# Performance work log

Measured on AMD Instinct MI355X. Metric: run time of the kernel, lower is better.

## Reference

```python
import jax, jax.numpy as jnp
import numpy as np

N_FIELDS = 8
N_NODES = 100000
N_EDGES = 6400000


def setup_inputs() -> dict:
    key = jax.random.key(0)
    k1, k2, k3, k4, k5 = jax.random.split(key, 5)
    q = jax.random.normal(k1, (N_FIELDS, N_NODES), dtype=jnp.float32)
    edges = jax.random.normal(k2, (N_EDGES, 1), dtype=jnp.float32)
    senders = jax.random.randint(k3, (N_EDGES,), 0, N_NODES, dtype=jnp.int32)
    receivers = jax.random.randint(k4, (N_EDGES,), 0, N_NODES, dtype=jnp.int32)
    dt = jax.random.uniform(k5, (1,), dtype=jnp.float32)
    # learned parameters, initialized exactly as in DeltaQGNN.__init__
    w_self = jnp.linspace(0.05, 0.09, N_FIELDS)
    w_msg = jnp.linspace(0.02, 0.04, N_FIELDS)
    w_edge = jnp.linspace(0.01, 0.03, N_FIELDS)
    b = jnp.linspace(0.005, 0.008, N_FIELDS)
    return {"q": q, "edges": edges, "senders": senders, "receivers": receivers,
            "dt": dt, "w_self": w_self, "w_msg": w_msg, "w_edge": w_edge, "b": b}


def reference(q, edges, senders, receivers, dt, w_self, w_msg, w_edge, b):
    # q: [F, N], edges: [E, 1], senders/receivers: [E], dt: [1]
    n_nodes = q.shape[1]
    edge_scalar = edges[:, 0]                                    # [E]
    # gather sender values for all fields at once: [F, E]
    msg_in = q[:, senders] + w_edge[:, None] * edge_scalar[None, :]
    # scatter-add to receivers per field: [F, N]
    msg = jax.vmap(lambda m: jax.ops.segment_sum(m, receivers, num_segments=n_nodes))(msg_in)
    rhs = w_self[:, None] * q + w_msg[:, None] * msg + b[:, None]
    return dt * rhs                                              # [F, N]
```

## Files before the change

kernel.cpp:

```cpp
#include <hip/hip_runtime.h>

#define NF 8
#define BSHIFT 8
#define BNODES 256
#define MAXNB 512
#define TPB 256
#define TPR 512
#define TPBF 1024
#define CHUNKF 6144
#define KPE 6
#define NBLKF 512
#define CAPB 17408
#define SPLIT 8
#define CAP 24
#define IDXSTR 26
#define LSLICE 2560

__global__ void k_transpose(const float* __restrict__ q, float* __restrict__ qT,
                            float* __restrict__ govf, unsigned* __restrict__ gcur,
                            int n_nodes, int nb) {
    int n = blockIdx.x * blockDim.x + threadIdx.x;
    if (n < nb) gcur[n] = 0u;
    if (n >= n_nodes) return;
    float4 a, b;
    a.x = q[0 * n_nodes + n]; a.y = q[1 * n_nodes + n];
    a.z = q[2 * n_nodes + n]; a.w = q[3 * n_nodes + n];
    b.x = q[4 * n_nodes + n]; b.y = q[5 * n_nodes + n];
    b.z = q[6 * n_nodes + n]; b.w = q[7 * n_nodes + n];
    float4* dst = reinterpret_cast<float4*>(qT + (size_t)n * NF);
    dst[0] = a; dst[1] = b;
    float* o = govf + (size_t)n * 9;
#pragma unroll
    for (int k = 0; k < 9; ++k) o[k] = 0.f;
}

__global__ __launch_bounds__(TPBF) void k_scatter_fused(
        const float* __restrict__ edges, const int* __restrict__ senders,
        const int* __restrict__ receivers, int n_edges, int nb, int tiles,
        unsigned* __restrict__ gcur, const float* __restrict__ qT,
        float* __restrict__ govf, uint2* __restrict__ rec) {
    __shared__ uint2 lrec[CHUNKF];
    __shared__ unsigned short lbkt[CHUNKF];
    __shared__ unsigned hist[MAXNB];
    __shared__ unsigned lbase[MAXNB];
    __shared__ unsigned gbase[MAXNB];

    for (int t = blockIdx.x; t < tiles; t += gridDim.x) {
        int start = t * CHUNKF;
        int end = min(start + CHUNKF, n_edges);
        int n = end - start;

        for (int i = threadIdx.x; i < nb; i += TPBF) hist[i] = 0u;
        __syncthreads();

        unsigned rcx[KPE], rcy[KPE], meta[KPE];
#pragma unroll
        for (int k = 0; k < KPE; ++k) {
            int i = (int)threadIdx.x + k * TPBF;
            meta[k] = 0xFFFFFFFFu;
            if (i < n) {
                int e = start + i;
                int s = senders[e];
                int r = receivers[e];
                float ev = edges[e];
                unsigned bkt = (unsigned)r >> BSHIFT;
                unsigned p = atomicAdd(&hist[bkt], 1u);
                rcx[k] = ((unsigned)(r & (BNODES - 1)) << 17) | (unsigned)s;
                rcy[k] = __float_as_uint(ev);
                meta[k] = (p << 9) | bkt;
            }
        }
        __syncthreads();

        if (threadIdx.x < (unsigned)nb)
            gbase[threadIdx.x] = atomicAdd(&gcur[threadIdx.x], hist[threadIdx.x]);
        if (threadIdx.x < 64) {
            int lane = threadIdx.x;
            unsigned carry = 0;
            for (int base = 0; base < nb; base += 64) {
                int bi = base + lane;
                unsigned v = (bi < nb) ? hist[bi] : 0u;
                unsigned x = v;
                for (int d = 1; d < 64; d <<= 1) {
                    unsigned y = __shfl_up(x, d, 64);
                    if (lane >= d) x += y;
                }
                if (bi < nb) lbase[bi] = carry + x - v;
                carry += __shfl(x, 63, 64);
            }
        }
        __syncthreads();

#pragma unroll
        for (int k = 0; k < KPE; ++k) {
            if (meta[k] != 0xFFFFFFFFu) {
                unsigned bkt = meta[k] & 0x1FFu;
                unsigned p   = meta[k] >> 9;
                unsigned slot = lbase[bkt] + p;
                lrec[slot] = make_uint2(rcx[k], rcy[k]);
                lbkt[slot] = (unsigned short)bkt;
            }
        }
        __syncthreads();

        for (int j = threadIdx.x; j < n; j += TPBF) {
            unsigned bkt = lbkt[j];
            uint2 rc = lrec[j];
            unsigned off = gbase[bkt] + ((unsigned)j - lbase[bkt]);
            if (off < CAPB) {
                rec[(size_t)bkt * CAPB + off] = rc;
            } else {
                unsigned snd = rc.x & 0x1FFFFu;
                unsigned rl = rc.x >> 17;
                float ev = __uint_as_float(rc.y);
                const float4* qs = reinterpret_cast<const float4*>(qT + (size_t)snd * NF);
                float4 q0 = qs[0];
                float4 q1 = qs[1];
                float* a = govf + ((size_t)bkt * BNODES + rl) * 9;
                atomicAdd(a + 0, q0.x); atomicAdd(a + 1, q0.y);
                atomicAdd(a + 2, q0.z); atomicAdd(a + 3, q0.w);
                atomicAdd(a + 4, q1.x); atomicAdd(a + 5, q1.y);
                atomicAdd(a + 6, q1.z); atomicAdd(a + 7, q1.w);
                atomicAdd(a + 8, ev);
            }
        }
        __syncthreads();
    }
}

__global__ __launch_bounds__(TPR) void k_reduce_slot(
        const uint2* __restrict__ rec, const unsigned* __restrict__ gcur,
        const float* __restrict__ qT, float* __restrict__ part,
        float* __restrict__ govf, int n_nodes) {
    __shared__ uint2 lrec[LSLICE];
    __shared__ unsigned short idx[BNODES * IDXSTR];
    __shared__ unsigned cur[BNODES];
    int t = threadIdx.x;
    if (t < BNODES) cur[t] = 0;
    __syncthreads();

    int bkt = blockIdx.x / SPLIT;
    int s   = blockIdx.x % SPLIT;
    unsigned len = gcur[bkt];
    if (len > CAPB) len = CAPB;
    size_t base = (size_t)bkt * CAPB;
    unsigned a0 = (unsigned)(((unsigned long long)len * s) / SPLIT);
    unsigned a1 = (unsigned)(((unsigned long long)len * (s + 1)) / SPLIT);
    unsigned slice = a1 - a0;

    for (unsigned i = t; i < slice; i += TPR) {
        uint2 rc = rec[base + a0 + i];
        if (i < LSLICE) lrec[i] = rc;
        unsigned rl = rc.x >> 17;
        unsigned pos = atomicAdd(&cur[rl], 1u);
        if (pos < CAP) {
            idx[rl * IDXSTR + pos] = (unsigned short)i;
        } else {
            unsigned snd = rc.x & 0x1FFFFu;
            float ev = __uint_as_float(rc.y);
            const float4* qs = reinterpret_cast<const float4*>(qT + (size_t)snd * NF);
            float4 q0 = qs[0];
            float4 q1 = qs[1];
            float* a = govf + ((size_t)bkt * BNODES + rl) * 9;
            atomicAdd(a + 0, q0.x); atomicAdd(a + 1, q0.y);
            atomicAdd(a + 2, q0.z); atomicAdd(a + 3, q0.w);
            atomicAdd(a + 4, q1.x); atomicAdd(a + 5, q1.y);
            atomicAdd(a + 6, q1.z); atomicAdd(a + 7, q1.w);
            atomicAdd(a + 8, ev);
        }
    }
    __syncthreads();

    int node = t >> 1;
    int parity = t & 1;
    float m[9];
#pragma unroll
    for (int k = 0; k < 9; ++k) m[k] = 0.f;
    unsigned cntv = cur[node];
    if (cntv > CAP) cntv = CAP;
    for (unsigned j = parity; j < cntv; j += 2) {
        unsigned i0 = idx[node * IDXSTR + j];
        uint2 rc0 = (i0 < LSLICE) ? lrec[i0] : rec[base + a0 + i0];
        const float4* qs0 = reinterpret_cast<const float4*>(qT + (size_t)(rc0.x & 0x1FFFFu) * NF);
        float4 a0v = qs0[0], a1v = qs0[1];
        m[0] += a0v.x; m[1] += a0v.y; m[2] += a0v.z; m[3] += a0v.w;
        m[4] += a1v.x; m[5] += a1v.y; m[6] += a1v.z; m[7] += a1v.w;
        m[8] += __uint_as_float(rc0.y);
    }
    __syncthreads();

    float* scratch = reinterpret_cast<float*>(lrec);
    if (parity == 1) {
        float* d = scratch + (size_t)node * 9;
#pragma unroll
        for (int k = 0; k < 9; ++k) d[k] = m[k];
    }
    __syncthreads();
    if (parity == 0) {
        const float* p2 = scratch + (size_t)node * 9;
        float* dst = part + (size_t)blockIdx.x * (BNODES * 9) + (size_t)node * 9;
#pragma unroll
        for (int k = 0; k < 9; ++k) dst[k] = m[k] + p2[k];
    }
}

__global__ void k_finalize2(const float* __restrict__ part, const float* __restrict__ govf,
                            const float* __restrict__ q,
                            const float* __restrict__ dtp, const float* __restrict__ w_self,
                            const float* __restrict__ w_msg, const float* __restrict__ w_edge,
                            const float* __restrict__ bv, float* __restrict__ out,
                            int split, int n_nodes) {
    int n = blockIdx.x * blockDim.x + threadIdx.x;
    if (n >= n_nodes) return;
    int bkt = n >> BSHIFT;
    int rl = n & (BNODES - 1);
    float m[9];
#pragma unroll
    for (int f = 0; f < 9; ++f) m[f] = govf[(size_t)n * 9 + f];
    for (int s = 0; s < split; ++s) {
        const float* p = part + ((size_t)(bkt * split + s) * BNODES + rl) * 9;
#pragma unroll
        for (int f = 0; f < 9; ++f) m[f] += p[f];
    }
    float dtv = dtp[0];
    float evs = m[8];
#pragma unroll
    for (int f = 0; f < NF; ++f) {
        float msg = m[f] + w_edge[f] * evs;
        out[(size_t)f * n_nodes + n] =
            dtv * (w_self[f] * q[(size_t)f * n_nodes + n] + w_msg[f] * msg + bv[f]);
    }
}

__global__ void k_transpose_zero(const float* __restrict__ q, float* __restrict__ qT,
                                 float* __restrict__ msgT, int n_nodes) {
    int n = blockIdx.x * blockDim.x + threadIdx.x;
    if (n >= n_nodes) return;
    float v[NF];
#pragma unroll
    for (int f = 0; f < NF; ++f) v[f] = q[f * n_nodes + n];
    float4* dst = reinterpret_cast<float4*>(qT + (size_t)n * NF);
    dst[0] = make_float4(v[0], v[1], v[2], v[3]);
    dst[1] = make_float4(v[4], v[5], v[6], v[7]);
    float4 z = make_float4(0.f, 0.f, 0.f, 0.f);
    float4* m = reinterpret_cast<float4*>(msgT + (size_t)n * NF);
    m[0] = z; m[1] = z;
}

__global__ void k_edge_scatter(const float* __restrict__ edges, const int* __restrict__ senders,
                               const int* __restrict__ receivers, const float* __restrict__ qT,
                               float* __restrict__ msgT, const float* __restrict__ w_edge,
                               int n_edges) {
    float we[NF];
#pragma unroll
    for (int f = 0; f < NF; ++f) we[f] = w_edge[f];
    int idx = blockIdx.x * blockDim.x + threadIdx.x;
    int stride = gridDim.x * blockDim.x;
    for (int e = idx; e < n_edges; e += stride) {
        int s = senders[e];
        int r = receivers[e];
        float ev = edges[e];
        const float4* qs = reinterpret_cast<const float4*>(qT + (size_t)s * NF);
        float4 q0 = qs[0];
        float4 q1 = qs[1];
        float* m = msgT + (size_t)r * NF;
        atomicAdd(m + 0, q0.x + we[0] * ev);
        atomicAdd(m + 1, q0.y + we[1] * ev);
        atomicAdd(m + 2, q0.z + we[2] * ev);
        atomicAdd(m + 3, q0.w + we[3] * ev);
        atomicAdd(m + 4, q1.x + we[4] * ev);
        atomicAdd(m + 5, q1.y + we[5] * ev);
        atomicAdd(m + 6, q1.z + we[6] * ev);
        atomicAdd(m + 7, q1.w + we[7] * ev);
    }
}

__global__ void k_finalize(const float* __restrict__ q, const float* __restrict__ msgT,
                           const float* __restrict__ dt, const float* __restrict__ w_self,
                           const float* __restrict__ w_msg, const float* __restrict__ b,
                           float* __restrict__ out, int n_nodes) {
    int n = blockIdx.x * blockDim.x + threadIdx.x;
    if (n >= n_nodes) return;
    float dtv = dt[0];
    const float4* m4 = reinterpret_cast<const float4*>(msgT + (size_t)n * NF);
    float4 m0 = m4[0];
    float4 m1 = m4[1];
    float mv[NF] = {m0.x, m0.y, m0.z, m0.w, m1.x, m1.y, m1.z, m1.w};
#pragma unroll
    for (int f = 0; f < NF; ++f) {
        out[f * n_nodes + n] = dtv * (w_self[f] * q[f * n_nodes + n] + w_msg[f] * mv[f] + b[f]);
    }
}

extern "C" void kernel_launch(void* const* d_in, const int* in_sizes, int n_in,
                              void* d_out, int out_size, void* d_ws, size_t ws_size,
                              hipStream_t stream) {
    const float* q         = (const float*)d_in[0];
    const float* edges     = (const float*)d_in[1];
    const int*   senders   = (const int*)d_in[2];
    const int*   receivers = (const int*)d_in[3];
    const float* dt        = (const float*)d_in[4];
    const float* w_self    = (const float*)d_in[5];
    const float* w_msg     = (const float*)d_in[6];
    const float* w_edge    = (const float*)d_in[7];
    const float* b         = (const float*)d_in[8];
    float* out = (float*)d_out;

    const int n_nodes = in_sizes[0] / NF;
    const int n_edges = in_sizes[2];
    const int nb = (n_nodes + BNODES - 1) >> BSHIFT;
    const int tiles = (n_edges + CHUNKF - 1) / CHUNKF;

    size_t rec_bytes  = (size_t)nb * CAPB * 8;
    size_t qT_bytes   = (size_t)n_nodes * NF * 4;
    size_t gcur_bytes = 256 + (size_t)nb * 4;
    size_t govf_bytes = (size_t)nb * BNODES * 9 * 4;
    size_t part_bytes = (size_t)SPLIT * nb * BNODES * 9 * 4;
    size_t need = rec_bytes + qT_bytes + gcur_bytes + govf_bytes + part_bytes + 1024;

    double mean_per_bucket = (double)n_edges / (double)nb;
    bool ok = (n_nodes <= 131072) && (nb <= MAXNB) && (need <= ws_size) &&
              (mean_per_bucket + 8.0 * __builtin_sqrt(mean_per_bucket) < (double)CAPB);

    if (ok) {
        char* p = (char*)d_ws;
        uint2*    rec  = (uint2*)p;    p += rec_bytes;
        float*    qT   = (float*)p;    p += qT_bytes;
        unsigned* gcur = (unsigned*)p; p += gcur_bytes;
        float*    govf = (float*)p;    p += govf_bytes;
        float*    part = (float*)(((uintptr_t)p + 255) & ~(uintptr_t)255);

        int nblk_f = tiles < NBLKF ? tiles : NBLKF;

        k_transpose<<<(n_nodes + TPB - 1) / TPB, TPB, 0, stream>>>(q, qT, govf, gcur,
                                                                   n_nodes, nb);
        k_scatter_fused<<<nblk_f, TPBF, 0, stream>>>(edges, senders, receivers, n_edges,
                                                     nb, tiles, gcur, qT, govf, rec);
        k_reduce_slot<<<nb * SPLIT, TPR, 0, stream>>>(rec, gcur, qT, part, govf, n_nodes);
        k_finalize2<<<(n_nodes + TPB - 1) / TPB, TPB, 0, stream>>>(
            part, govf, q, dt, w_self, w_msg, w_edge, b, out, SPLIT, n_nodes);
    } else {
        float* qT   = (float*)d_ws;
        float* msgT = qT + (size_t)n_nodes * NF;
        k_transpose_zero<<<(n_nodes + TPB - 1) / TPB, TPB, 0, stream>>>(q, qT, msgT, n_nodes);
        k_edge_scatter<<<3072, TPB, 0, stream>>>(edges, senders, receivers, qT, msgT,
                                                 w_edge, n_edges);
        k_finalize<<<(n_nodes + TPB - 1) / TPB, TPB, 0, stream>>>(q, msgT, dt, w_self, w_msg,
                                                                  b, out, n_nodes);
    }
}
```

Measured before the change: 108.6 us.

## Stage reduce-slot records via direct global-to-LDS loads and retune scatter blocks

The reduce kernel now copies each slice's records into shared memory with the asynchronous global_load_lds builtin in 1 KB wave chunks before processing, instead of loading them through registers and storing them to LDS inside the loop. Slice boundaries are rounded to even indices so the 16-byte copies stay aligned, and the last slice takes the remainder. The scatter kernel is retuned to smaller blocks with smaller chunks and more blocks, and the workspace padding grows. The copy can read up to one 1 KB chunk past the slice end, which relies on that padding and adds a full barrier before processing.

```diff
diff --git a/kernel.cpp b/kernel.cpp
--- a/kernel.cpp
+++ b/kernel.cpp
@@ -6,10 +6,10 @@
 #define MAXNB 512
 #define TPB 256
 #define TPR 512
-#define TPBF 1024
-#define CHUNKF 6144
+#define TPBF 512
+#define CHUNKF 3072
 #define KPE 6
-#define NBLKF 512
+#define NBLKF 1024
 #define CAPB 17408
 #define SPLIT 8
 #define CAP 24
@@ -132,25 +132,59 @@
         const uint2* __restrict__ rec, const unsigned* __restrict__ gcur,
         const float* __restrict__ qT, float* __restrict__ part,
         float* __restrict__ govf, int n_nodes) {
-    __shared__ uint2 lrec[LSLICE];
+    __shared__ __align__(16) uint2 lrec[LSLICE];
     __shared__ unsigned short idx[BNODES * IDXSTR];
     __shared__ unsigned cur[BNODES];
     int t = threadIdx.x;
     if (t < BNODES) cur[t] = 0;
-    __syncthreads();
 
     int bkt = blockIdx.x / SPLIT;
     int s   = blockIdx.x % SPLIT;
     unsigned len = gcur[bkt];
     if (len > CAPB) len = CAPB;
     size_t base = (size_t)bkt * CAPB;
-    unsigned a0 = (unsigned)(((unsigned long long)len * s) / SPLIT);
-    unsigned a1 = (unsigned)(((unsigned long long)len * (s + 1)) / SPLIT);
+    unsigned a0 = ((unsigned)(((unsigned long long)len * s) / SPLIT)) & ~1u;
+    unsigned a1 = (s + 1 == SPLIT) ? len
+                : ((unsigned)(((unsigned long long)len * (s + 1)) / SPLIT)) & ~1u;
     unsigned slice = a1 - a0;
-
-    for (unsigned i = t; i < slice; i += TPR) {
+    unsigned staged = slice < LSLICE ? slice : LSLICE;
+
+    {
+        int wid = t >> 6, lane = t & 63;
+        unsigned ncalls = (staged * 8u + 1023u) >> 10;
+        const char* g0 = (const char*)(rec + base + a0);
+        for (unsigned c = wid; c < ncalls; c += TPR / 64) {
+            const char* g = g0 + (size_t)c * 1024 + (size_t)lane * 16;
+            char* l = (char*)lrec + (size_t)c * 1024;
+            __builtin_amdgcn_global_load_lds(
+                (const __attribute__((address_space(1))) void*)g,
+                (__attribute__((address_space(3))) void*)l, 16, 0, 0);
+        }
+    }
+    __syncthreads();
+
+    for (unsigned i = t; i < staged; i += TPR) {
+        uint2 rc = lrec[i];
+        unsigned rl = rc.x >> 17;
+        unsigned pos = atomicAdd(&cur[rl], 1u);
+        if (pos < CAP) {
+            idx[rl * IDXSTR + pos] = (unsigned short)i;
+        } else {
+            unsigned snd = rc.x & 0x1FFFFu;
+            float ev = __uint_as_float(rc.y);
+            const float4* qs = reinterpret_cast<const float4*>(qT + (size_t)snd * NF);
+            float4 q0 = qs[0];
+            float4 q1 = qs[1];
+            float* a = govf + ((size_t)bkt * BNODES + rl) * 9;
+            atomicAdd(a + 0, q0.x); atomicAdd(a + 1, q0.y);
+            atomicAdd(a + 2, q0.z); atomicAdd(a + 3, q0.w);
+            atomicAdd(a + 4, q1.x); atomicAdd(a + 5, q1.y);
+            atomicAdd(a + 6, q1.z); atomicAdd(a + 7, q1.w);
+            atomicAdd(a + 8, ev);
+        }
+    }
+    for (unsigned i = LSLICE + t; i < slice; i += TPR) {
         uint2 rc = rec[base + a0 + i];
-        if (i < LSLICE) lrec[i] = rc;
         unsigned rl = rc.x >> 17;
         unsigned pos = atomicAdd(&cur[rl], 1u);
         if (pos < CAP) {
@@ -316,7 +350,7 @@
     size_t gcur_bytes = 256 + (size_t)nb * 4;
     size_t govf_bytes = (size_t)nb * BNODES * 9 * 4;
     size_t part_bytes = (size_t)SPLIT * nb * BNODES * 9 * 4;
-    size_t need = rec_bytes + qT_bytes + gcur_bytes + govf_bytes + part_bytes + 1024;
+    size_t need = rec_bytes + qT_bytes + gcur_bytes + govf_bytes + part_bytes + 4096;
 
     double mean_per_bucket = (double)n_edges / (double)nb;
     bool ok = (n_nodes <= 131072) && (nb <= MAXNB) && (need <= ws_size) &&
```

Result: slower. 123.4 us (+13.7%).
